# Kernel tuning notes

Measured on AMD Instinct MI355X. Metric: run time of the kernel, lower is better.

## Reference

```python
import jax, jax.numpy as jnp
import numpy as np

B, T, D, H = 4, 1024, 1024, 16
DH = D // H  # 64

def setup_inputs() -> dict:
    key = jax.random.key(0)
    ks = jax.random.split(key, 5)
    s = 1.0 / np.sqrt(D)
    return {
        "x": jax.random.normal(ks[0], (B, T, D), dtype=jnp.float32),
        "Wqkv": jax.random.uniform(ks[1], (D, 3 * D), dtype=jnp.float32, minval=-s, maxval=s),
        "bqkv": jax.random.uniform(ks[2], (3 * D,), dtype=jnp.float32, minval=-s, maxval=s),
        "Wproj": jax.random.uniform(ks[3], (D, D), dtype=jnp.float32, minval=-s, maxval=s),
        "bproj": jax.random.uniform(ks[4], (D,), dtype=jnp.float32, minval=-s, maxval=s),
        "mask": jnp.ones((B, T), dtype=jnp.int32),
    }

def reference(x, Wqkv, bqkv, Wproj, bproj, mask):
    Bx, Tx, C = x.shape
    qkv = x @ Wqkv + bqkv                      # [B,T,3D]
    q, k, v = jnp.split(qkv, 3, axis=-1)
    # [B,H,T,DH]
    q = q.reshape(Bx, Tx, H, DH).transpose(0, 2, 1, 3)
    k = k.reshape(Bx, Tx, H, DH).transpose(0, 2, 1, 3)
    v = v.reshape(Bx, Tx, H, DH).transpose(0, 2, 1, 3)
    att = jnp.einsum("bhqd,bhkd->bhqk", q, k) / np.sqrt(DH)
    causal = jnp.tril(jnp.ones((Tx, Tx), dtype=bool))          # [T,T]
    keep = causal[None, None] & (mask[:, None, None, :] != 0)  # [B,1,T,T] broadcast
    att = jnp.where(keep, att, -jnp.inf)
    att = jax.nn.softmax(att, axis=-1)
    # dropout is identity in eval / p=0
    out = jnp.einsum("bhqk,bhkd->bhqd", att, v)                # [B,H,T,DH]
    out = out.transpose(0, 2, 1, 3).reshape(Bx, Tx, C)
    return out @ Wproj + bproj
```

## Files before the change

### kernel.cpp

```cpp
#include <hip/hip_runtime.h>
#include <hip/hip_bf16.h>
#include <cstddef>
#include <cstdint>

#define Bb 4
#define Tt 1024
#define Dd 1024
#define Hh 16

typedef __bf16 bf16x8 __attribute__((ext_vector_type(8)));
typedef __bf16 bf16x4 __attribute__((ext_vector_type(4)));
typedef float  f32x4  __attribute__((ext_vector_type(4)));

__device__ __forceinline__ void gload16(const void* g, void* l) {
    __builtin_amdgcn_global_load_lds(
        (const __attribute__((address_space(1))) void*)g,
        (__attribute__((address_space(3))) void*)l, 16, 0, 0);
}

__global__ __launch_bounds__(256) void prep(const float* __restrict__ x,
                                            const float* __restrict__ Wqkv,
                                            const float* __restrict__ Wproj,
                                            __bf16* __restrict__ xb,
                                            __bf16* __restrict__ wqT,
                                            __bf16* __restrict__ wpT) {
    const int bid = blockIdx.x;
    if (bid < 4096) {
        int i = bid * 256 + threadIdx.x;
        float4 v = ((const float4*)x)[i];
        bf16x4 o = { (__bf16)v.x, (__bf16)v.y, (__bf16)v.z, (__bf16)v.w };
        ((bf16x4*)xb)[i] = o;
        return;
    }
    __shared__ float ld[64][65];
    const float* in;
    __bf16* out;
    int K, N, k0, n0;
    if (bid < 4096 + 768) {
        int j = bid - 4096;
        in = Wqkv; out = wqT; K = 1024; N = 3072;
        k0 = (j & 15) * 64; n0 = (j >> 4) * 64;
    } else {
        int j = bid - 4096 - 768;
        in = Wproj; out = wpT; K = 1024; N = 1024;
        k0 = (j & 15) * 64; n0 = (j >> 4) * 64;
    }
    #pragma unroll
    for (int i = 0; i < 16; i++) {
        int idx = i * 256 + threadIdx.x;
        int r = idx >> 6, c = idx & 63;
        ld[r][c] = in[(size_t)(k0 + r) * N + n0 + c];
    }
    __syncthreads();
    #pragma unroll
    for (int i = 0; i < 16; i++) {
        int idx = i * 256 + threadIdx.x;
        int r = idx >> 6, c = idx & 63;
        out[(size_t)(n0 + r) * K + k0 + c] = (__bf16)ld[c][r];
    }
}

__global__ __launch_bounds__(256) void gemm_qkv(const __bf16* __restrict__ A,
                                                const __bf16* __restrict__ Bt,
                                                const float* __restrict__ bias,
                                                __bf16* __restrict__ Cout,
                                                __bf16* __restrict__ vt,
                                                int M, int N, int K) {
    __shared__ __align__(16) __bf16 smem[17408];
    __bf16* const As = smem;
    __bf16* const Bs = smem + 8192;

    const int tid  = threadIdx.x;
    const int lane = tid & 63;
    const int wave = tid >> 6;
    const int wy = wave >> 1, wx = wave & 1;
    const int l15 = lane & 15, quad = lane >> 4;
    const size_t row0 = (size_t)blockIdx.y * 128;
    const size_t col0 = (size_t)blockIdx.x * 128;

    f32x4 acc[4][4] = {};

    #pragma unroll
    for (int i = 0; i < 2; i++) {
        int c = i * 256 + tid;
        int r = c >> 2, seg = (c & 3) ^ ((r >> 1) & 3);
        gload16(&A[(row0 + r) * K + seg * 8], &As[c * 8]);
        gload16(&Bt[(col0 + r) * K + seg * 8], &Bs[c * 8]);
    }

    const int niter = K >> 5;
    for (int it = 0; it < niter; it++) {
        __syncthreads();
        const int cur = it & 1;
        if (it + 1 < niter) {
            const int k0 = (it + 1) << 5;
            #pragma unroll
            for (int i = 0; i < 2; i++) {
                int c = i * 256 + tid;
                int r = c >> 2, seg = (c & 3) ^ ((r >> 1) & 3);
                gload16(&A[(row0 + r) * K + k0 + seg * 8], &As[(cur ^ 1) * 4096 + c * 8]);
                gload16(&Bt[(col0 + r) * K + k0 + seg * 8], &Bs[(cur ^ 1) * 4096 + c * 8]);
            }
        }
        bf16x8 af[4], bfr[4];
        #pragma unroll
        for (int i = 0; i < 4; i++) {
            const int r = wy * 64 + i * 16 + l15;
            af[i] = *(const bf16x8*)&As[cur * 4096 + r * 32 + ((quad ^ ((r >> 1) & 3)) * 8)];
        }
        #pragma unroll
        for (int j = 0; j < 4; j++) {
            const int r = wx * 64 + j * 16 + l15;
            bfr[j] = *(const bf16x8*)&Bs[cur * 4096 + r * 32 + ((quad ^ ((r >> 1) & 3)) * 8)];
        }
        #pragma unroll
        for (int i = 0; i < 4; i++)
            #pragma unroll
            for (int j = 0; j < 4; j++)
                acc[i][j] = __builtin_amdgcn_mfma_f32_16x16x32_bf16(af[i], bfr[j], acc[i][j], 0, 0, 0);
    }

    __syncthreads();
    #pragma unroll
    for (int j = 0; j < 4; j++) {
        const int cl = wx * 64 + j * 16 + l15;
        const size_t col = col0 + cl;
        const float bj = bias[col];
        const float scale = (col < 1024) ? 0.125f : 1.0f;
        #pragma unroll
        for (int i = 0; i < 4; i++) {
            const int rl = wy * 64 + i * 16 + quad * 4;
            #pragma unroll
            for (int r = 0; r < 4; r++)
                smem[(rl + r) * 132 + cl] = (__bf16)((acc[i][j][r] + bj) * scale);
        }
    }
    __syncthreads();
    #pragma unroll
    for (int p = 0; p < 8; p++) {
        const int row = p * 16 + (tid >> 4);
        const int ch  = tid & 15;
        bf16x8 v = *(const bf16x8*)&smem[row * 132 + ch * 8];
        *(bf16x8*)&Cout[(row0 + row) * N + col0 + ch * 8] = v;
    }
    if (col0 >= 2048) {
        const int bidx = (int)(row0 >> 10);
        const int t0g  = (int)(row0 & 1023);
        const int cl   = tid >> 1;
        const int half = tid & 1;
        const int hd   = (int)(col0 - 2048) + cl;
        const size_t vrow = ((size_t)((bidx * Hh + (hd >> 6)) * 64 + (hd & 63))) * Tt + t0g;
        #pragma unroll
        for (int s = 0; s < 8; s++) {
            const int t = half * 64 + s * 8;
            bf16x8 v;
            #pragma unroll
            for (int u = 0; u < 8; u++) v[u] = smem[(t + u) * 132 + cl];
            *(bf16x8*)&vt[vrow + t] = v;
        }
    }
}

__global__ __launch_bounds__(256) void gemm_bf16_n64(const __bf16* __restrict__ A,
                                                     const __bf16* __restrict__ Bt,
                                                     const float* __restrict__ bias,
                                                     float* __restrict__ Cout,
                                                     int M, int N, int K) {
    __shared__ __align__(16) __bf16 As[128 * 64];
    __shared__ __align__(16) __bf16 Bs[64 * 64];
    const int tid  = threadIdx.x;
    const int lane = tid & 63;
    const int wave = tid >> 6;
    const int wy = wave >> 1, wx = wave & 1;
    const int l15 = lane & 15, quad = lane >> 4;
    const size_t row0 = (size_t)blockIdx.y * 128;
    const size_t col0 = (size_t)blockIdx.x * 64;

    f32x4 acc[4][2] = {};

    for (int k0 = 0; k0 < K; k0 += 64) {
        #pragma unroll
        for (int i = 0; i < 4; i++) {
            int c = i * 256 + tid;
            int r = c >> 3, seg = (c & 7) ^ (r & 7);
            gload16(&A[(row0 + r) * K + k0 + seg * 8], &As[c * 8]);
        }
        #pragma unroll
        for (int i = 0; i < 2; i++) {
            int c = i * 256 + tid;
            int r = c >> 3, seg = (c & 7) ^ (r & 7);
            gload16(&Bt[(col0 + r) * K + k0 + seg * 8], &Bs[c * 8]);
        }
        __syncthreads();
        #pragma unroll
        for (int kc = 0; kc < 2; kc++) {
            bf16x8 af[4], bfr[2];
            #pragma unroll
            for (int i = 0; i < 4; i++)
                af[i] = *(const bf16x8*)&As[(wy * 64 + i * 16 + l15) * 64 +
                                            (((kc * 4 + quad) ^ (l15 & 7)) * 8)];
            #pragma unroll
            for (int j = 0; j < 2; j++)
                bfr[j] = *(const bf16x8*)&Bs[(wx * 32 + j * 16 + l15) * 64 +
                                             (((kc * 4 + quad) ^ (l15 & 7)) * 8)];
            #pragma unroll
            for (int i = 0; i < 4; i++)
                #pragma unroll
                for (int j = 0; j < 2; j++)
                    acc[i][j] = __builtin_amdgcn_mfma_f32_16x16x32_bf16(af[i], bfr[j], acc[i][j], 0, 0, 0);
        }
        __syncthreads();
    }

    #pragma unroll
    for (int j = 0; j < 2; j++) {
        const size_t col = col0 + wx * 32 + j * 16 + l15;
        const float bj = bias[col];
        #pragma unroll
        for (int i = 0; i < 4; i++) {
            const size_t row = row0 + wy * 64 + i * 16 + quad * 4;
            #pragma unroll
            for (int r = 0; r < 4; r++)
                Cout[(row + r) * N + col] = acc[i][j][r] + bj;
        }
    }
}

__global__ __launch_bounds__(256, 4) void attn_mfma(const __bf16* __restrict__ qkv,
                                                    const __bf16* __restrict__ vt,
                                                    const int* __restrict__ mask,
                                                    __bf16* __restrict__ att) {
    __shared__ __align__(16) __bf16 Ks[2][4096];
    __shared__ __align__(16) __bf16 Vs[2][4096];
    __shared__ __align__(16) __bf16 Ps[4][1024];

    const int h  = blockIdx.x & 15;
    const int b  = blockIdx.x >> 4;
    const int qt = 15 - blockIdx.y;
    const int tid = threadIdx.x, lane = tid & 63, wave = tid >> 6;
    const int l15 = lane & 15, quad = lane >> 4;

    #pragma unroll
    for (int i = 0; i < 2; i++) {
        int c = i * 256 + tid;
        int rr = c >> 3, ch = c & 7;
        gload16(&qkv[((size_t)(b * Tt + qt * 64 + rr)) * 3072 + h * 64 + ((ch ^ (rr & 7)) * 8)],
                &Ks[0][c * 8]);
    }

    uint32_t mlo = 0, mhi = 0;
    for (int p = 0; p < 16; p++) {
        unsigned long long bal = __ballot(mask[b * Tt + p * 64 + lane] != 0);
        if ((lane & 15) == p) { mlo = (uint32_t)bal; mhi = (uint32_t)(bal >> 32); }
    }

    __syncthreads();
    bf16x8 qf0 = *(const bf16x8*)&Ks[0][(wave * 16 + l15) * 64 + ((quad ^ (l15 & 7)) * 8)];
    bf16x8 qf1 = *(const bf16x8*)&Ks[0][(wave * 16 + l15) * 64 + (((4 + quad) ^ (l15 & 7)) * 8)];
    __syncthreads();

    #pragma unroll
    for (int i = 0; i < 2; i++) {
        int c = i * 256 + tid;
        int rr = c >> 3, ch = c & 7, sw = ((ch ^ (rr & 7)) * 8);
        gload16(&qkv[((size_t)(b * Tt + rr)) * 3072 + 1024 + h * 64 + sw], &Ks[0][c * 8]);
        gload16(&vt[((size_t)((b * Hh + h) * 64 + rr)) * Tt + sw], &Vs[0][c * 8]);
    }

    f32x4 Oacc[4] = {};
    float lsum = 0.0f;

    for (int kt = 0; kt <= qt; kt++) {
        __syncthreads();
        const int cur = kt & 1;
        if (kt < qt) {
            #pragma unroll
            for (int i = 0; i < 2; i++) {
                int c = i * 256 + tid;
                int rr = c >> 3, ch = c & 7, sw = ((ch ^ (rr & 7)) * 8);
                gload16(&qkv[((size_t)(b * Tt + (kt + 1) * 64 + rr)) * 3072 + 1024 + h * 64 + sw],
                        &Ks[cur ^ 1][c * 8]);
                gload16(&vt[((size_t)((b * Hh + h) * 64 + rr)) * Tt + (kt + 1) * 64 + sw],
                        &Vs[cur ^ 1][c * 8]);
            }
        }

        const uint32_t lo = (uint32_t)__builtin_amdgcn_readlane((int)mlo, kt);
        const uint32_t hi = (uint32_t)__builtin_amdgcn_readlane((int)mhi, kt);

        bf16x8 ak[4][2];
        #pragma unroll
        for (int j = 0; j < 4; j++)
            #pragma unroll
            for (int kc = 0; kc < 2; kc++)
                ak[j][kc] = *(const bf16x8*)&Ks[cur][(j * 16 + l15) * 64 +
                                                     (((kc * 4 + quad) ^ (l15 & 7)) * 8)];
        #pragma unroll
        for (int j = 0; j < 4; j++) {
            f32x4 st = {};
            st = __builtin_amdgcn_mfma_f32_16x16x32_bf16(ak[j][0], qf0, st, 0, 0, 0);
            st = __builtin_amdgcn_mfma_f32_16x16x32_bf16(ak[j][1], qf1, st, 0, 0, 0);
            const uint32_t fld = (j < 2) ? (lo >> (j * 16)) : (hi >> ((j - 2) * 16));
            bf16x4 pv;
            #pragma unroll
            for (int r = 0; r < 4; r++) {
                const int tloc = j * 16 + quad * 4 + r;
                bool keep = (fld >> (quad * 4 + r)) & 1;
                if (kt == qt) keep = keep && (tloc <= wave * 16 + l15);
                const float pe = keep ? __expf(st[r]) : 0.0f;
                lsum += pe;
                pv[r] = (__bf16)pe;
            }
            *(bf16x4*)&Ps[wave][l15 * 64 + (((j * 4 + quad) ^ ((l15 & 7) << 1)) * 4)] = pv;
        }

        bf16x8 av[4][2];
        #pragma unroll
        for (int n = 0; n < 4; n++)
            #pragma unroll
            for (int kc = 0; kc < 2; kc++)
                av[n][kc] = *(const bf16x8*)&Vs[cur][(n * 16 + l15) * 64 +
                                                     (((kc * 4 + quad) ^ (l15 & 7)) * 8)];
        bf16x8 p0 = *(const bf16x8*)&Ps[wave][l15 * 64 + (((2 * quad) ^ ((l15 & 7) << 1)) * 4)];
        bf16x8 p1 = *(const bf16x8*)&Ps[wave][l15 * 64 + (((2 * (4 + quad)) ^ ((l15 & 7) << 1)) * 4)];
        #pragma unroll
        for (int n = 0; n < 4; n++) {
            Oacc[n] = __builtin_amdgcn_mfma_f32_16x16x32_bf16(av[n][0], p0, Oacc[n], 0, 0, 0);
            Oacc[n] = __builtin_amdgcn_mfma_f32_16x16x32_bf16(av[n][1], p1, Oacc[n], 0, 0, 0);
        }
    }

    float lt = lsum;
    lt += __shfl_xor(lt, 16);
    lt += __shfl_xor(lt, 32);
    const float inv = 1.0f / lt;
    const int q = qt * 64 + wave * 16 + l15;
    #pragma unroll
    for (int n = 0; n < 4; n++) {
        bf16x4 o;
        #pragma unroll
        for (int r = 0; r < 4; r++) o[r] = (__bf16)(Oacc[n][r] * inv);
        *(bf16x4*)&att[((size_t)(b * Tt + q)) * Dd + h * 64 + n * 16 + quad * 4] = o;
    }
}

extern "C" void kernel_launch(void* const* d_in, const int* in_sizes, int n_in,
                              void* d_out, int out_size, void* d_ws, size_t ws_size,
                              hipStream_t stream) {
    const float* x     = (const float*)d_in[0];
    const float* Wqkv  = (const float*)d_in[1];
    const float* bqkv  = (const float*)d_in[2];
    const float* Wproj = (const float*)d_in[3];
    const float* bproj = (const float*)d_in[4];
    const int*   mask  = (const int*)d_in[5];
    float* out = (float*)d_out;

    __bf16* xb  = (__bf16*)d_ws;
    __bf16* wqT = xb  + (size_t)4096 * 1024;
    __bf16* wpT = wqT + (size_t)3072 * 1024;
    __bf16* qkv = wpT + (size_t)1024 * 1024;
    __bf16* vt  = qkv + (size_t)4096 * 3072;
    __bf16* att = vt  + (size_t)4 * 16 * 64 * 1024;

    prep<<<4096 + 768 + 256, 256, 0, stream>>>(x, Wqkv, Wproj, xb, wqT, wpT);

    gemm_qkv<<<dim3(24, 32), 256, 0, stream>>>(xb, wqT, bqkv, qkv, vt, 4096, 3072, 1024);

    attn_mfma<<<dim3(64, 16), 256, 0, stream>>>(qkv, vt, mask, att);

    gemm_bf16_n64<<<dim3(16, 32), 256, 0, stream>>>(att, wpT, bproj, out, 4096, 1024, 1024);
}
```

Before: 163.5 us.

## Remap GEMM blocks for XCD-local L2 reuse and split V transpose into its own kernel

Both GEMMs now use a 1D grid and remap block IDs so that blocks landing on the same XCD (id & 7) cover neighbouring column tiles. This is meant to improve L2 reuse of the shared A and B tiles across the MI355X chiplets. The V transpose epilogue is removed from gemm_qkv and moved into a separate v_transpose kernel that reads the V slice of qkv back from global memory. That shortens the GEMM epilogue but adds a kernel launch and an extra read and write of V.

Result: no change. 165.5 us (+1.2%).

```diff
diff --git a/kernel.cpp b/kernel.cpp
--- a/kernel.cpp
+++ b/kernel.cpp
@@ -60,23 +60,50 @@
     }
 }
 
+__global__ __launch_bounds__(256) void v_transpose(const __bf16* __restrict__ qkv,
+                                                   __bf16* __restrict__ vt) {
+    __shared__ __bf16 ld[64][65];
+    const int t0 = blockIdx.x * 64;
+    const int h  = blockIdx.y;
+    const int b  = blockIdx.z;
+    const size_t src = ((size_t)(b * Tt + t0)) * 3072 + 2048 + h * 64;
+    #pragma unroll
+    for (int i = 0; i < 16; i++) {
+        int idx = i * 256 + threadIdx.x;
+        int tr = idx >> 6, dc = idx & 63;
+        ld[tr][dc] = qkv[src + (size_t)tr * 3072 + dc];
+    }
+    __syncthreads();
+    const size_t dst = ((size_t)((b * Hh + h) * 64)) * Tt + t0;
+    #pragma unroll
+    for (int i = 0; i < 16; i++) {
+        int idx = i * 256 + threadIdx.x;
+        int dr = idx >> 6, tc = idx & 63;
+        vt[dst + (size_t)dr * Tt + tc] = ld[tc][dr];
+    }
+}
+
 __global__ __launch_bounds__(256) void gemm_qkv(const __bf16* __restrict__ A,
                                                 const __bf16* __restrict__ Bt,
                                                 const float* __restrict__ bias,
                                                 __bf16* __restrict__ Cout,
-                                                __bf16* __restrict__ vt,
                                                 int M, int N, int K) {
     __shared__ __align__(16) __bf16 smem[17408];
     __bf16* const As = smem;
     __bf16* const Bs = smem + 8192;
+
+    const int id = blockIdx.x;
+    const int cxcd = id & 7, rr_ = id >> 3;
+    const int bx = cxcd * 3 + (rr_ % 3);
+    const int by = rr_ / 3;
 
     const int tid  = threadIdx.x;
     const int lane = tid & 63;
     const int wave = tid >> 6;
     const int wy = wave >> 1, wx = wave & 1;
     const int l15 = lane & 15, quad = lane >> 4;
-    const size_t row0 = (size_t)blockIdx.y * 128;
-    const size_t col0 = (size_t)blockIdx.x * 128;
+    const size_t row0 = (size_t)by * 128;
+    const size_t col0 = (size_t)bx * 128;
 
     f32x4 acc[4][4] = {};
 
@@ -142,22 +169,6 @@
         const int ch  = tid & 15;
         bf16x8 v = *(const bf16x8*)&smem[row * 132 + ch * 8];
         *(bf16x8*)&Cout[(row0 + row) * N + col0 + ch * 8] = v;
-    }
-    if (col0 >= 2048) {
-        const int bidx = (int)(row0 >> 10);
-        const int t0g  = (int)(row0 & 1023);
-        const int cl   = tid >> 1;
-        const int half = tid & 1;
-        const int hd   = (int)(col0 - 2048) + cl;
-        const size_t vrow = ((size_t)((bidx * Hh + (hd >> 6)) * 64 + (hd & 63))) * Tt + t0g;
-        #pragma unroll
-        for (int s = 0; s < 8; s++) {
-            const int t = half * 64 + s * 8;
-            bf16x8 v;
-            #pragma unroll
-            for (int u = 0; u < 8; u++) v[u] = smem[(t + u) * 132 + cl];
-            *(bf16x8*)&vt[vrow + t] = v;
-        }
     }
 }
 
@@ -168,13 +179,19 @@
                                                      int M, int N, int K) {
     __shared__ __align__(16) __bf16 As[128 * 64];
     __shared__ __align__(16) __bf16 Bs[64 * 64];
+
+    const int id = blockIdx.x;
+    const int cxcd = id & 7, rr_ = id >> 3;
+    const int bx = cxcd * 2 + (rr_ & 1);
+    const int by = rr_ >> 1;
+
     const int tid  = threadIdx.x;
     const int lane = tid & 63;
     const int wave = tid >> 6;
     const int wy = wave >> 1, wx = wave & 1;
     const int l15 = lane & 15, quad = lane >> 4;
-    const size_t row0 = (size_t)blockIdx.y * 128;
-    const size_t col0 = (size_t)blockIdx.x * 64;
+    const size_t row0 = (size_t)by * 128;
+    const size_t col0 = (size_t)bx * 64;
 
     f32x4 acc[4][2] = {};
 
@@ -364,9 +381,10 @@
 
     prep<<<4096 + 768 + 256, 256, 0, stream>>>(x, Wqkv, Wproj, xb, wqT, wpT);
 
-    gemm_qkv<<<dim3(24, 32), 256, 0, stream>>>(xb, wqT, bqkv, qkv, vt, 4096, 3072, 1024);
-
+    gemm_qkv<<<768, 256, 0, stream>>>(xb, wqT, bqkv, qkv, 4096, 3072, 1024);
+
+    v_transpose<<<dim3(16, 16, 4), 256, 0, stream>>>(qkv, vt);
     attn_mfma<<<dim3(64, 16), 256, 0, stream>>>(qkv, vt, mask, att);
 
-    gemm_bf16_n64<<<dim3(16, 32), 256, 0, stream>>>(att, wpT, bproj, out, 4096, 1024, 1024);
-}
+    gemm_bf16_n64<<<512, 256, 0, stream>>>(att, wpT, bproj, out, 4096, 1024, 1024);
+}
```
